# Kernel tuning notes

Measured on AMD Instinct MI355X. Metric: run time of the kernel, lower is better.

Reference implementation:

```python
import jax, jax.numpy as jnp
import numpy as np

B = 64
NS = [5024, 1257, 315, 80, 21]  # padded vertex counts per mesh level
K = 9                            # spiral length
LAT = 256


def _sconv(x, idx, W, b, elu=True):
    # x: [B, N, F], idx: [N, K] spiral neighbor indices -> gather, GEMM, activation, zero-pad mask
    Bq, N, _ = x.shape
    g = x[:, idx.reshape(-1), :].reshape(Bq, N, -1)  # [B, N, K*F]
    o = g @ W + b
    if elu:
        o = jax.nn.elu(o)
    return o.at[:, -1, :].set(0.0)  # zero the padding vertex


def _pool(M, x):
    # M: [M_out, M_in] dense down/up-sample matrix
    return jnp.einsum('mn,bnf->bmf', M, x)


def _forward(x, s0, s1, s2, s3, D0, D1, D2, D3, U0, U1, U2, U3,
             We0, be0, We1, be1, We2, be2, We3, be3,
             fceW, fceb, fcdW, fcdb,
             Wd0, bd0, Wd1, bd1, Wd2, bd2, Wd3, bd3):
    # encoder: spiral conv + downsample at each level
    h = _pool(D0, _sconv(x, s0, We0, be0))
    h = _pool(D1, _sconv(h, s1, We1, be1))
    h = _pool(D2, _sconv(h, s2, We2, be2))
    h = _pool(D3, _sconv(h, s3, We3, be3))
    z = h.reshape(h.shape[0], -1) @ fceW + fceb          # [B, LAT]
    # decoder: upsample + spiral conv, last conv has identity activation
    h = (z @ fcdW + fcdb).reshape(z.shape[0], NS[4], -1)  # [B, 21, 256]
    h = _sconv(_pool(U3, h), s3, Wd0, bd0)
    h = _sconv(_pool(U2, h), s2, Wd1, bd1)
    h = _sconv(_pool(U1, h), s1, Wd2, bd2)
    h = _sconv(_pool(U0, h), s0, Wd3, bd3, elu=False)
    return h  # [B, 5024, 3]


def setup_inputs() -> dict:
    key = jax.random.key(0)
    ks = iter(jax.random.split(key, 64))
    nrm = lambda shape, s=0.05: jax.random.normal(next(ks), shape, dtype=jnp.float32) * s
    d = {}
    d['x'] = jax.random.normal(next(ks), (B, NS[0], 3), dtype=jnp.float32)
    for i in range(4):
        n = NS[i]
        d[f's{i}'] = jax.random.randint(next(ks), (n, K), 0, n, dtype=jnp.int32).astype(jnp.int64)
    for i in range(4):
        d[f'D{i}'] = nrm((NS[i + 1], NS[i]))
        d[f'U{i}'] = nrm((NS[i], NS[i + 1]))
    enc = [(3, 64), (64, 64), (64, 128), (128, 256)]
    for i, (fi, fo) in enumerate(enc):
        d[f'We{i}'] = nrm((fi * K, fo))
        d[f'be{i}'] = jnp.zeros((fo,), jnp.float32)
    d['fceW'] = nrm((NS[4] * 256, LAT))
    d['fceb'] = jnp.zeros((LAT,), jnp.float32)
    d['fcdW'] = nrm((LAT, NS[4] * 256))
    d['fcdb'] = jnp.zeros((NS[4] * 256,), jnp.float32)
    dec = [(256, 128), (128, 64), (64, 64), (64, 3)]
    for i, (fi, fo) in enumerate(dec):
        d[f'Wd{i}'] = nrm((fi * K, fo))
        d[f'bd{i}'] = jnp.zeros((fo,), jnp.float32)
    return d


def reference(x, s0, s1, s2, s3, D0, D1, D2, D3, U0, U1, U2, U3,
              We0, be0, We1, be1, We2, be2, We3, be3,
              fceW, fceb, fcdW, fcdb,
              Wd0, bd0, Wd1, bd1, Wd2, bd2, Wd3, bd3):
    return _forward(x, s0, s1, s2, s3, D0, D1, D2, D3, U0, U1, U2, U3,
                    We0, be0, We1, be1, We2, be2, We3, be3,
                    fceW, fceb, fcdW, fcdb,
                    Wd0, bd0, Wd1, bd1, Wd2, bd2, Wd3, bd3)
```

## Files before the change

### kernel.cpp

```cpp
#include <hip/hip_runtime.h>
#include <math.h>

typedef __attribute__((ext_vector_type(8))) _Float16 half8;
typedef __attribute__((ext_vector_type(4))) float f32x4;
typedef unsigned long long u64;

#define BK 32

#define EPI_NAT  0
#define EPI_TR   1
#define EPI_FCD  2
#define EPI_OUT  3
#define EPI_PART 4

typedef const __attribute__((address_space(1))) void* gas1;
typedef __attribute__((address_space(3))) void* las3;

__device__ __forceinline__ void gl16(const void* g, void* l) {
    __builtin_amdgcn_global_load_lds((gas1)g, (las3)l, 16, 0, 0);
}
template<int N> __device__ __forceinline__ void vwait() {
    asm volatile("s_waitcnt vmcnt(%0)" :: "n"(N) : "memory");
}
__device__ __forceinline__ void barx() {
    asm volatile("" ::: "memory");
    __builtin_amdgcn_s_barrier();
    asm volatile("" ::: "memory");
}

__global__ void __launch_bounds__(256, 3) pool2_k_impl();

template<int TBM>
__global__ __launch_bounds__(256, 3) void pool2_k(
    const _Float16* __restrict__ Aw, const _Float16* __restrict__ Bw,
    _Float16* __restrict__ Cp, int M, int Np, u64 c_rs)
{
    constexpr int FM  = TBM / 32;
    constexpr int LPS = TBM / 64 + 2;

    __shared__ _Float16 sA[3][TBM][BK];
    __shared__ _Float16 sB[3][128][BK];

    const int t  = threadIdx.x;
    const int m0 = blockIdx.y * TBM;
    const int f0 = blockIdx.x * 128;
    const int lane = t & 63;
    const int wid  = t >> 6;
    const int wm = wid >> 1;
    const int wf = wid & 1;
    const int lm = lane & 15;
    const int lg = lane >> 4;

    f32x4 acc[FM][4];
    #pragma unroll
    for (int i = 0; i < FM; ++i)
        #pragma unroll
        for (int j = 0; j < 4; ++j)
            acc[i][j] = (f32x4)0.0f;

    auto stage = [&](int buf, int ks) {
        #pragma unroll
        for (int j = 0; j < TBM / 64; ++j) {
            int c   = t + j * 256;
            int row = c >> 2;
            int sw  = ((c & 3) ^ ((row >> 1) & 3)) * 8;
            int rc  = m0 + row; if (rc >= M) rc = M - 1;
            gl16(Aw + (u64)rc * Np + ks * BK + sw,
                 (_Float16*)&sA[buf][0][0] + (u64)c * 8);
        }
        #pragma unroll
        for (int j = 0; j < 2; ++j) {
            int c   = t + j * 256;
            int row = c >> 2;
            int sw  = ((c & 3) ^ ((row >> 1) & 3)) * 8;
            gl16(Bw + (u64)(f0 + row) * Np + ks * BK + sw,
                 (_Float16*)&sB[buf][0][0] + (u64)c * 8);
        }
    };

    auto compute = [&](int buf) {
        const int sa = (lg ^ ((lm >> 1) & 3)) * 8;
        half8 af[FM], bf[4];
        #pragma unroll
        for (int i = 0; i < FM; ++i)
            af[i] = *(const half8*)&sA[buf][wm * (FM * 16) + i * 16 + lm][sa];
        #pragma unroll
        for (int j = 0; j < 4; ++j)
            bf[j] = *(const half8*)&sB[buf][wf * 64 + j * 16 + lm][sa];
        #pragma unroll
        for (int i = 0; i < FM; ++i)
            #pragma unroll
            for (int j = 0; j < 4; ++j)
                acc[i][j] = __builtin_amdgcn_mfma_f32_16x16x32_f16(af[i], bf[j], acc[i][j], 0, 0, 0);
    };

    const int ke = Np / BK;
    stage(0, 0);
    if (1 < ke) stage(1, 1);
    if (2 < ke) stage(2, 2);
    int cur = 0;
    for (int ks = 0; ks < ke; ++ks) {
        int rem = ke - ks;
        if (rem >= 3)      vwait<2 * LPS>();
        else if (rem == 2) vwait<LPS>();
        else               vwait<0>();
        barx();
        compute(cur);
        barx();
        if (ks + 3 < ke) stage(cur, ks + 3);
        cur = (cur == 2) ? 0 : cur + 1;
    }

    #pragma unroll
    for (int j = 0; j < 4; ++j) {
        int fl = f0 + wf * 64 + j * 16 + lm;
        #pragma unroll
        for (int i = 0; i < FM; ++i) {
            #pragma unroll
            for (int r = 0; r < 4; ++r) {
                int m = m0 + wm * (FM * 16) + i * 16 + lg * 4 + r;
                if (m < M)
                    Cp[(u64)m * c_rs + fl] = (_Float16)acc[i][j][r];
            }
        }
    }
}

template<int AMODE, int EPI, int TBM, int TBF, int WM, int WF>
__global__ __launch_bounds__(256) void gemm_k(
    const _Float16* __restrict__ Aw, u64 a_rs,
    const int* __restrict__ idx, int FiLog,
    const _Float16* __restrict__ Bw,
    const float* __restrict__ bias,
    void* __restrict__ Cp, u64 c_rs, int Mp_out,
    int M, int Np, int F, int flags, int ksp)
{
    constexpr int FM = TBM / WM / 16;
    constexpr int FF = TBF / WF / 16;
    constexpr int LPS_A = TBM / 64;
    constexpr bool BSM = (TBF < 64);
    constexpr int LPS_B = BSM ? 0 : TBF / 64;
    constexpr int LW0 = LPS_A + (BSM ? 1 : LPS_B);
    constexpr int LWX = LPS_A + LPS_B;
    constexpr int NI = (AMODE == 1) ? TBM : 2;

    __shared__ _Float16 sA[3][TBM][BK];
    __shared__ _Float16 sB[3][TBF][BK];
    __shared__ int sIdx[NI][9];

    const int t  = threadIdx.x;
    const int b  = blockIdx.z;
    const int m0 = blockIdx.y * TBM;
    const int f0 = blockIdx.x * TBF;
    const int lane = t & 63;
    const int wid  = t >> 6;
    const int wm = wid / WF;
    const int wf = wid % WF;
    const int lm = lane & 15;
    const int lg = lane >> 4;
    const int Fi = 1 << FiLog;

    f32x4 acc[FM][FF];
    #pragma unroll
    for (int i = 0; i < FM; ++i)
        #pragma unroll
        for (int j = 0; j < FF; ++j)
            acc[i][j] = (f32x4)0.0f;

    if constexpr (AMODE == 1) {
        for (int i = t; i < TBM * 9; i += 256) {
            int r = i / 9, k = i - r * 9;
            int rc = m0 + r; if (rc >= M) rc = M - 1;
            sIdx[r][k] = idx[rc * 9 + k];
        }
        __syncthreads();
    } else if constexpr (AMODE == 5) {
        if (t < 18) {
            int r = t / 9, k = t - r * 9;
            sIdx[r][k] = idx[((m0 >> 6) + r) * 9 + k];
        }
        __syncthreads();
    }

    auto stage = [&](int buf, int ks) {
        if constexpr (AMODE != 2) {
            #pragma unroll
            for (int j = 0; j < LPS_A; ++j) {
                int c   = t + j * 256;
                int row = c >> 2;
                int sw  = ((c & 3) ^ ((row >> 1) & 3)) * 8;
                int col = ks * BK + sw;
                const _Float16* src;
                if constexpr (AMODE == 3) {
                    int rc = m0 + row; if (rc >= M) rc = M - 1;
                    src = Aw + (u64)rc * Np + col;
                } else if constexpr (AMODE == 1) {
                    int k = col >> FiLog, fi = col & (Fi - 1);
                    src = Aw + (u64)sIdx[row][k] * a_rs + b * Fi + fi;
                } else if constexpr (AMODE == 4) {
                    int k = col >> FiLog, fi = col & (Fi - 1);
                    src = Aw + (u64)k * a_rs + (m0 + row) * Fi + fi;
                } else {
                    int k = col >> FiLog, fi = col & (Fi - 1);
                    int bb = (m0 + row) & 63;
                    src = Aw + (u64)sIdx[row >> 6][k] * a_rs + bb * Fi + fi;
                }
                gl16(src, &sA[buf][row][(c & 3) * 8]);
            }
        }
        if constexpr (!BSM) {
            #pragma unroll
            for (int j = 0; j < LPS_B; ++j) {
                int c   = t + j * 256;
                int row = c >> 2;
                int sw  = ((c & 3) ^ ((row >> 1) & 3)) * 8;
                gl16(Bw + (u64)(f0 + row) * Np + ks * BK + sw, &sB[buf][row][(c & 3) * 8]);
            }
        } else {
            if (wid == 0) {
                int c   = t;
                int row = c >> 2;
                int sw  = ((c & 3) ^ ((row >> 1) & 3)) * 8;
                gl16(Bw + (u64)(f0 + row) * Np + ks * BK + sw, &sB[buf][row][(c & 3) * 8]);
            }
        }
    };

    auto compute = [&](int buf) {
        const int sa = (lg ^ ((lm >> 1) & 3)) * 8;
        half8 af[FM], bf[FF];
        #pragma unroll
        for (int i = 0; i < FM; ++i)
            af[i] = *(const half8*)&sA[buf][wm * (FM * 16) + i * 16 + lm][sa];
        #pragma unroll
        for (int j = 0; j < FF; ++j)
            bf[j] = *(const half8*)&sB[buf][wf * (FF * 16) + j * 16 + lm][sa];
        #pragma unroll
        for (int i = 0; i < FM; ++i)
            #pragma unroll
            for (int j = 0; j < FF; ++j)
                acc[i][j] = __builtin_amdgcn_mfma_f32_16x16x32_f16(af[i], bf[j], acc[i][j], 0, 0, 0);
    };

    if constexpr (AMODE == 2) {
        stage(0, 0);
        {
            int row = t >> 1;
            int base = (t & 1) * 16;
            int rg = m0 + row;
            #pragma unroll
            for (int q = 0; q < 16; ++q) {
                int n = base + q;
                _Float16 val = (_Float16)0.f;
                if (rg < M && n < 27) {
                    int k = n / 3, fi = n - k * 3;
                    val = Aw[(u64)idx[rg * 9 + k] * a_rs + b * 3 + fi];
                }
                int ch = (n >> 3) ^ ((row >> 1) & 3);
                sA[0][row][ch * 8 + (n & 7)] = val;
            }
        }
        __syncthreads();
        compute(0);
    } else {
        int kb = 0, ke = Np / BK;
        if constexpr (AMODE == 4) { kb = b * ksp; ke = kb + ksp; }
        stage(0, kb);
        if (kb + 1 < ke) stage(1, kb + 1);
        if (kb + 2 < ke) stage(2, kb + 2);
        int cur = 0;
        for (int ks = kb; ks < ke; ++ks) {
            int rem = ke - ks;
            if (rem >= 3) {
                if constexpr (LW0 == LWX) vwait<2 * LW0>();
                else { if (wid == 0) vwait<2 * LW0>(); else vwait<2 * LWX>(); }
            } else if (rem == 2) {
                if constexpr (LW0 == LWX) vwait<LW0>();
                else { if (wid == 0) vwait<LW0>(); else vwait<LWX>(); }
            } else {
                vwait<0>();
            }
            barx();
            compute(cur);
            barx();
            if (ks + 3 < ke) stage(cur, ks + 3);
            cur = (cur == 2) ? 0 : cur + 1;
        }
    }

    #pragma unroll
    for (int j = 0; j < FF; ++j) {
        int fl = f0 + wf * (FF * 16) + j * 16 + lm;
        float bv = 0.f;
        if (bias != nullptr && fl < F) bv = bias[fl];
        #pragma unroll
        for (int i = 0; i < FM; ++i) {
            #pragma unroll
            for (int r = 0; r < 4; ++r) {
                int m = m0 + wm * (FM * 16) + i * 16 + lg * 4 + r;
                float v = acc[i][j][r] + bv;
                if (flags & 1) v = (v > 0.f) ? v : expm1f(v);
                if constexpr (EPI == EPI_NAT) {
                    if (m < M && fl < F)
                        ((_Float16*)Cp)[(u64)m * c_rs + fl] = (_Float16)v;
                } else if constexpr (EPI == EPI_TR) {
                    if (m < Mp_out && fl < F) {
                        float o = (m < M && !((flags & 2) && m == M - 1)) ? v : 0.f;
                        ((_Float16*)Cp)[(u64)b * c_rs + (u64)fl * Mp_out + m] = (_Float16)o;
                    }
                } else if constexpr (EPI == EPI_FCD) {
                    if (m < M && fl < F)
                        ((_Float16*)Cp)[((u64)m * 256 + (fl & 255)) * 32 + (fl >> 8)] = (_Float16)v;
                } else if constexpr (EPI == EPI_PART) {
                    if (m < M && fl < F)
                        ((float*)Cp)[(u64)b * c_rs + (u64)m * F + fl] = v;
                } else {
                    if (m < M && fl < F) {
                        int vo = m >> 6, bb = m & 63;
                        float o = ((flags & 2) && vo == Mp_out - 1) ? 0.f : v;
                        ((float*)Cp)[((u64)bb * Mp_out + vo) * 3 + fl] = o;
                    }
                }
            }
        }
    }
}

struct CvtPtrs { const float* p[18]; };

constexpr int CV_R[18]  = {1257,5024,315,1257,80,315,21,80,  64,64,128,256,256,5376,128,64,64,16};
constexpr int CV_N[18]  = {5024,1257,1257,315,315,80,80,21,  27,576,576,1152,5376,256,2304,1152,576,576};
constexpr int CV_NP[18] = {5120,1280,1280,320,320,96,96,32,  32,576,576,1152,5376,256,2304,1152,576,576};
constexpr int CV_F[18]  = {0,0,0,0,0,0,0,0,  64,64,128,256,256,5376,128,64,64,3};

constexpr u64 cv_elems(int i) { return (u64)CV_R[i] * CV_NP[i]; }
constexpr u64 cv_off(int i) { u64 o = 0; for (int j = 0; j < i; ++j) o += (cv_elems(j) + 255) & ~(u64)255; return o; }
constexpr int cv_blk(int i) { return (int)((cv_elems(i) + 255) >> 8); }
constexpr int cv_start(int i) { int s = 0; for (int j = 0; j < i; ++j) s += cv_blk(j); return s; }

__global__ __launch_bounds__(256) void cvt_all(CvtPtrs ps, _Float16* __restrict__ dst)
{
    const int bx = blockIdx.x, t = threadIdx.x;
    #pragma unroll
    for (int i = 0; i < 18; ++i) {
        if (bx >= cv_start(i) && bx < cv_start(i + 1)) {
            const u64 e = (u64)(bx - cv_start(i)) * 256 + t;
            if (e < cv_elems(i)) {
                const int NP = CV_NP[i], N = CV_N[i], Fo = CV_F[i];
                int row = (int)(e / (u64)NP);
                int col = (int)(e - (u64)row * NP);
                float v = 0.f;
                const float* s = ps.p[i];
                if (Fo == 0) { if (col < N) v = s[(u64)row * N + col]; }
                else         { if (col < N && row < Fo) v = s[(u64)col * Fo + row]; }
                dst[cv_off(i) + e] = (_Float16)v;
            }
        }
    }
}

__global__ void cvt_x(const float* __restrict__ src, _Float16* __restrict__ dst)
{
    int i = blockIdx.x * 256 + threadIdx.x;
    if (i >= 64 * 5024 * 3) return;
    int v = i / 192;
    int r = i - v * 192;
    int b = r / 3, c = r - b * 3;
    dst[i] = (_Float16)src[((u64)b * 5024 + v) * 3 + c];
}

__global__ void reduce_fce(const float* __restrict__ part, const float* __restrict__ bias,
                           _Float16* __restrict__ z)
{
    int i = blockIdx.x * 256 + threadIdx.x;
    int fl = i & 255;
    float s = bias[fl];
    #pragma unroll
    for (int p = 0; p < 8; ++p) s += part[(u64)p * 16384 + i];
    z[i] = (_Float16)s;
}

extern "C" void kernel_launch(void* const* d_in, const int* in_sizes, int n_in,
                              void* d_out, int out_size, void* d_ws, size_t ws_size,
                              hipStream_t stream)
{
    const float* x  = (const float*)d_in[0];
    const int* s0 = (const int*)d_in[1];
    const int* s1 = (const int*)d_in[2];
    const int* s2 = (const int*)d_in[3];
    const int* s3 = (const int*)d_in[4];
    const float* be0 = (const float*)d_in[14];
    const float* be1 = (const float*)d_in[16];
    const float* be2 = (const float*)d_in[18];
    const float* be3 = (const float*)d_in[20];
    const float* fceb = (const float*)d_in[22];
    const float* fcdb = (const float*)d_in[24];
    const float* bd0 = (const float*)d_in[26];
    const float* bd1 = (const float*)d_in[28];
    const float* bd2 = (const float*)d_in[30];
    const float* bd3 = (const float*)d_in[32];

    _Float16* W = (_Float16*)d_ws;
    size_t off = 0;
    auto alloc = [&](size_t e) { size_t o = off; off += (e + 255) & ~(size_t)255; return o; };

    const size_t oActV = alloc((size_t)5024 * 4096);
    const size_t oActT = alloc((size_t)4096 * 5120);
    const size_t oZ    = alloc((size_t)64 * 256);
    const size_t oPart = alloc((size_t)8 * 64 * 256 * 2);
    const size_t oU3in = alloc((size_t)16384 * 32);
    const size_t oXp   = alloc((size_t)5024 * 192);
    const size_t oCvt  = alloc((size_t)(cv_off(17) + ((cv_elems(17) + 255) & ~(u64)255)));
    auto wofs = [&](int i) { return oCvt + (size_t)cv_off(i); };

    cvt_x<<<dim3((64 * 5024 * 3 + 255) / 256), 256, 0, stream>>>(x, W + oXp);
    {
        CvtPtrs ps;
        ps.p[0] = (const float*)d_in[5];
        ps.p[1] = (const float*)d_in[6];
        ps.p[2] = (const float*)d_in[7];
        ps.p[3] = (const float*)d_in[8];
        ps.p[4] = (const float*)d_in[9];
        ps.p[5] = (const float*)d_in[10];
        ps.p[6] = (const float*)d_in[11];
        ps.p[7] = (const float*)d_in[12];
        ps.p[8] = (const float*)d_in[13];
        ps.p[9] = (const float*)d_in[15];
        ps.p[10] = (const float*)d_in[17];
        ps.p[11] = (const float*)d_in[19];
        ps.p[12] = (const float*)d_in[21];
        ps.p[13] = (const float*)d_in[23];
        ps.p[14] = (const float*)d_in[25];
        ps.p[15] = (const float*)d_in[27];
        ps.p[16] = (const float*)d_in[29];
        ps.p[17] = (const float*)d_in[31];
        cvt_all<<<dim3(cv_start(18)), 256, 0, stream>>>(ps, W + oCvt);
    }
    hipMemsetAsync(W + oU3in, 0, (size_t)16384 * 32 * sizeof(_Float16), stream);

    #define GEMM(AM, EP, BM_, BF_, WM_, WF_, gx, gy, gz, Aw_, ars_, idx_, FiL_, Bw_, bias_, Cp_, crs_, Mp_, M_, Np_, F_, fl_, ksp_) \
        gemm_k<AM, EP, BM_, BF_, WM_, WF_><<<dim3(gx, gy, gz), 256, 0, stream>>>( \
            Aw_, ars_, idx_, FiL_, Bw_, bias_, Cp_, crs_, Mp_, M_, Np_, F_, fl_, ksp_)
    #define POOL(TBM_, gx, gy, Aw_, Bw_, Cp_, M_, Np_, crs_) \
        pool2_k<TBM_><<<dim3(gx, gy), 256, 0, stream>>>(Aw_, Bw_, Cp_, M_, Np_, crs_)

    GEMM(2, EPI_TR, 128, 64, 2, 2, 1, 40, 64, W + oXp, 192, s0, 0,
         W + wofs(8), be0, W + oActT, (u64)64 * 5120, 5120, 5024, 32, 64, 3, 0);
    POOL(64, 32, 20, W + wofs(0), W + oActT, W + oActV, 1257, 5120, 4096);
    GEMM(1, EPI_TR, 128, 64, 2, 2, 1, 10, 64, W + oActV, 4096, s1, 6,
         W + wofs(9), be1, W + oActT, (u64)64 * 1280, 1280, 1257, 576, 64, 3, 0);
    POOL(64, 32, 5, W + wofs(2), W + oActT, W + oActV, 315, 1280, 4096);
    GEMM(1, EPI_TR, 128, 64, 2, 2, 2, 3, 64, W + oActV, 4096, s2, 6,
         W + wofs(10), be2, W + oActT, (u64)128 * 320, 320, 315, 576, 128, 3, 0);
    POOL(64, 64, 2, W + wofs(4), W + oActT, W + oActV, 80, 320, 8192);
    GEMM(1, EPI_TR, 128, 64, 2, 2, 4, 1, 64, W + oActV, 8192, s3, 7,
         W + wofs(11), be3, W + oActT, (u64)256 * 96, 96, 80, 1152, 256, 3, 0);
    POOL(64, 128, 1, W + wofs(6), W + oActT, W + oActV, 21, 96, 16384);
    GEMM(4, EPI_PART, 64, 64, 2, 2, 4, 1, 8, W + oActV, 16384, nullptr, 8,
         W + wofs(12), nullptr, W + oPart, (u64)64 * 256, 0, 64, 5376, 256, 0, 21);
    reduce_fce<<<dim3(64), 256, 0, stream>>>((const float*)(W + oPart), fceb, W + oZ);
    GEMM(3, EPI_FCD, 64, 128, 2, 2, 42, 1, 1, W + oZ, 0, nullptr, 0,
         W + wofs(13), fcdb, W + oU3in, 0, 0, 64, 256, 5376, 0, 0);
    POOL(64, 128, 2, W + wofs(7), W + oU3in, W + oActV, 80, 32, 16384);
    GEMM(1, EPI_TR, 128, 64, 2, 2, 2, 1, 64, W + oActV, 16384, s3, 8,
         W + wofs(14), bd0, W + oActT, (u64)128 * 96, 96, 80, 2304, 128, 3, 0);
    POOL(64, 64, 5, W + wofs(5), W + oActT, W + oActV, 315, 96, 8192);
    GEMM(1, EPI_TR, 128, 64, 2, 2, 1, 3, 64, W + oActV, 8192, s2, 7,
         W + wofs(15), bd1, W + oActT, (u64)64 * 320, 320, 315, 1152, 64, 3, 0);
    POOL(64, 32, 20, W + wofs(3), W + oActT, W + oActV, 1257, 320, 4096);
    GEMM(1, EPI_TR, 128, 64, 2, 2, 1, 10, 64, W + oActV, 4096, s1, 6,
         W + wofs(16), bd2, W + oActT, (u64)64 * 1280, 1280, 1257, 576, 64, 3, 0);
    POOL(128, 32, 40, W + wofs(1), W + oActT, W + oActV, 5024, 1280, 4096);
    GEMM(5, EPI_OUT, 128, 16, 4, 1, 1, 2512, 1, W + oActV, 4096, s0, 6,
         W + wofs(17), bd3, d_out, 0, 5024, 321536, 576, 3, 2, 0);
    #undef GEMM
    #undef POOL
}
```

Before: 572.2 us.

## Split-K the first two encoder pools and use 128-thread blocks for level-1 convs

Adds a split-K variant of the pool GEMM that writes fp32 partials, plus a reduction kernel that sums them and converts to fp16. It is used for the D0 and D1 downsample pools, which have long K and few output tiles. The spiral-conv GEMM is now templated on thread count, and the level-1 convs run with 128-thread blocks and a 2x1 warp layout. The goal is more blocks in flight on the small-grid stages, at the cost of extra partial-buffer traffic and an additional kernel launch per split pool.

```diff
diff --git a/kernel.cpp b/kernel.cpp
--- a/kernel.cpp
+++ b/kernel.cpp
@@ -2,6 +2,7 @@
 #include <math.h>
 
 typedef __attribute__((ext_vector_type(8))) _Float16 half8;
+typedef __attribute__((ext_vector_type(4))) _Float16 half4;
 typedef __attribute__((ext_vector_type(4))) float f32x4;
 typedef unsigned long long u64;
 
@@ -28,12 +29,10 @@
     asm volatile("" ::: "memory");
 }
 
-__global__ void __launch_bounds__(256, 3) pool2_k_impl();
-
-template<int TBM>
+template<int TBM, int SPLIT>
 __global__ __launch_bounds__(256, 3) void pool2_k(
     const _Float16* __restrict__ Aw, const _Float16* __restrict__ Bw,
-    _Float16* __restrict__ Cp, int M, int Np, u64 c_rs)
+    void* __restrict__ Cp, int M, int Np, u64 c_rs, int ksp, u64 pstr)
 {
     constexpr int FM  = TBM / 32;
     constexpr int LPS = TBM / 64 + 2;
@@ -94,12 +93,13 @@
                 acc[i][j] = __builtin_amdgcn_mfma_f32_16x16x32_f16(af[i], bf[j], acc[i][j], 0, 0, 0);
     };
 
-    const int ke = Np / BK;
-    stage(0, 0);
-    if (1 < ke) stage(1, 1);
-    if (2 < ke) stage(2, 2);
+    const int kb = blockIdx.z * ksp;
+    const int ke = kb + ksp;
+    stage(0, kb);
+    if (kb + 1 < ke) stage(1, kb + 1);
+    if (kb + 2 < ke) stage(2, kb + 2);
     int cur = 0;
-    for (int ks = 0; ks < ke; ++ks) {
+    for (int ks = kb; ks < ke; ++ks) {
         int rem = ke - ks;
         if (rem >= 3)      vwait<2 * LPS>();
         else if (rem == 2) vwait<LPS>();
@@ -119,15 +119,35 @@
             #pragma unroll
             for (int r = 0; r < 4; ++r) {
                 int m = m0 + wm * (FM * 16) + i * 16 + lg * 4 + r;
-                if (m < M)
-                    Cp[(u64)m * c_rs + fl] = (_Float16)acc[i][j][r];
-            }
-        }
-    }
-}
-
-template<int AMODE, int EPI, int TBM, int TBF, int WM, int WF>
-__global__ __launch_bounds__(256) void gemm_k(
+                if (m < M) {
+                    if constexpr (SPLIT > 1)
+                        ((float*)Cp)[(u64)blockIdx.z * pstr + (u64)m * c_rs + fl] = acc[i][j][r];
+                    else
+                        ((_Float16*)Cp)[(u64)m * c_rs + fl] = (_Float16)acc[i][j][r];
+                }
+            }
+        }
+    }
+}
+
+template<int P>
+__global__ __launch_bounds__(256) void reduce_pool(
+    const float* __restrict__ part, _Float16* __restrict__ out, int total4, u64 pstr4)
+{
+    int i = blockIdx.x * 256 + threadIdx.x;
+    if (i >= total4) return;
+    f32x4 s = ((const f32x4*)part)[i];
+    #pragma unroll
+    for (int p = 1; p < P; ++p) {
+        f32x4 v = ((const f32x4*)part)[(u64)p * pstr4 + i];
+        s = s + v;
+    }
+    half4 h = {(_Float16)s[0], (_Float16)s[1], (_Float16)s[2], (_Float16)s[3]};
+    ((half4*)out)[i] = h;
+}
+
+template<int AMODE, int EPI, int NT, int TBM, int TBF, int WM, int WF>
+__global__ __launch_bounds__(NT) void gemm_k(
     const _Float16* __restrict__ Aw, u64 a_rs,
     const int* __restrict__ idx, int FiLog,
     const _Float16* __restrict__ Bw,
@@ -137,9 +157,9 @@
 {
     constexpr int FM = TBM / WM / 16;
     constexpr int FF = TBF / WF / 16;
-    constexpr int LPS_A = TBM / 64;
+    constexpr int LPS_A = TBM * 4 / NT;
     constexpr bool BSM = (TBF < 64);
-    constexpr int LPS_B = BSM ? 0 : TBF / 64;
+    constexpr int LPS_B = BSM ? 0 : TBF * 4 / NT;
     constexpr int LW0 = LPS_A + (BSM ? 1 : LPS_B);
     constexpr int LWX = LPS_A + LPS_B;
     constexpr int NI = (AMODE == 1) ? TBM : 2;
@@ -168,7 +188,7 @@
             acc[i][j] = (f32x4)0.0f;
 
     if constexpr (AMODE == 1) {
-        for (int i = t; i < TBM * 9; i += 256) {
+        for (int i = t; i < TBM * 9; i += NT) {
             int r = i / 9, k = i - r * 9;
             int rc = m0 + r; if (rc >= M) rc = M - 1;
             sIdx[r][k] = idx[rc * 9 + k];
@@ -186,7 +206,7 @@
         if constexpr (AMODE != 2) {
             #pragma unroll
             for (int j = 0; j < LPS_A; ++j) {
-                int c   = t + j * 256;
+                int c   = t + j * NT;
                 int row = c >> 2;
                 int sw  = ((c & 3) ^ ((row >> 1) & 3)) * 8;
                 int col = ks * BK + sw;
@@ -211,7 +231,7 @@
         if constexpr (!BSM) {
             #pragma unroll
             for (int j = 0; j < LPS_B; ++j) {
-                int c   = t + j * 256;
+                int c   = t + j * NT;
                 int row = c >> 2;
                 int sw  = ((c & 3) ^ ((row >> 1) & 3)) * 8;
                 gl16(Bw + (u64)(f0 + row) * Np + ks * BK + sw, &sB[buf][row][(c & 3) * 8]);
@@ -408,6 +428,7 @@
     const size_t oActT = alloc((size_t)4096 * 5120);
     const size_t oZ    = alloc((size_t)64 * 256);
     const size_t oPart = alloc((size_t)8 * 64 * 256 * 2);
+    const size_t oPP   = alloc((size_t)2 * 1257 * 4096 * 2);
     const size_t oU3in = alloc((size_t)16384 * 32);
     const size_t oXp   = alloc((size_t)5024 * 192);
     const size_t oCvt  = alloc((size_t)(cv_off(17) + ((cv_elems(17) + 255) & ~(u64)255)));
@@ -438,40 +459,46 @@
     }
     hipMemsetAsync(W + oU3in, 0, (size_t)16384 * 32 * sizeof(_Float16), stream);
 
-    #define GEMM(AM, EP, BM_, BF_, WM_, WF_, gx, gy, gz, Aw_, ars_, idx_, FiL_, Bw_, bias_, Cp_, crs_, Mp_, M_, Np_, F_, fl_, ksp_) \
-        gemm_k<AM, EP, BM_, BF_, WM_, WF_><<<dim3(gx, gy, gz), 256, 0, stream>>>( \
+    #define GEMM(AM, EP, NT_, BM_, BF_, WM_, WF_, gx, gy, gz, Aw_, ars_, idx_, FiL_, Bw_, bias_, Cp_, crs_, Mp_, M_, Np_, F_, fl_, ksp_) \
+        gemm_k<AM, EP, NT_, BM_, BF_, WM_, WF_><<<dim3(gx, gy, gz), NT_, 0, stream>>>( \
             Aw_, ars_, idx_, FiL_, Bw_, bias_, Cp_, crs_, Mp_, M_, Np_, F_, fl_, ksp_)
     #define POOL(TBM_, gx, gy, Aw_, Bw_, Cp_, M_, Np_, crs_) \
-        pool2_k<TBM_><<<dim3(gx, gy), 256, 0, stream>>>(Aw_, Bw_, Cp_, M_, Np_, crs_)
-
-    GEMM(2, EPI_TR, 128, 64, 2, 2, 1, 40, 64, W + oXp, 192, s0, 0,
+        pool2_k<TBM_, 1><<<dim3(gx, gy, 1), 256, 0, stream>>>(Aw_, Bw_, (void*)(Cp_), M_, Np_, crs_, (Np_) / BK, 0)
+
+    GEMM(2, EPI_TR, 256, 128, 64, 2, 2, 1, 40, 64, W + oXp, 192, s0, 0,
          W + wofs(8), be0, W + oActT, (u64)64 * 5120, 5120, 5024, 32, 64, 3, 0);
-    POOL(64, 32, 20, W + wofs(0), W + oActT, W + oActV, 1257, 5120, 4096);
-    GEMM(1, EPI_TR, 128, 64, 2, 2, 1, 10, 64, W + oActV, 4096, s1, 6,
+    pool2_k<128, 2><<<dim3(32, 10, 2), 256, 0, stream>>>(
+        W + wofs(0), W + oActT, (void*)(W + oPP), 1257, 5120, 4096, 80, (u64)1257 * 4096);
+    reduce_pool<2><<<dim3((1257 * 1024 + 255) / 256), 256, 0, stream>>>(
+        (const float*)(W + oPP), W + oActV, 1257 * 1024, (u64)1257 * 1024);
+    GEMM(1, EPI_TR, 128, 128, 64, 2, 1, 1, 10, 64, W + oActV, 4096, s1, 6,
          W + wofs(9), be1, W + oActT, (u64)64 * 1280, 1280, 1257, 576, 64, 3, 0);
-    POOL(64, 32, 5, W + wofs(2), W + oActT, W + oActV, 315, 1280, 4096);
-    GEMM(1, EPI_TR, 128, 64, 2, 2, 2, 3, 64, W + oActV, 4096, s2, 6,
+    pool2_k<64, 2><<<dim3(32, 5, 2), 256, 0, stream>>>(
+        W + wofs(2), W + oActT, (void*)(W + oPP), 315, 1280, 4096, 20, (u64)315 * 4096);
+    reduce_pool<2><<<dim3((315 * 1024 + 255) / 256), 256, 0, stream>>>(
+        (const float*)(W + oPP), W + oActV, 315 * 1024, (u64)315 * 1024);
+    GEMM(1, EPI_TR, 256, 128, 64, 2, 2, 2, 3, 64, W + oActV, 4096, s2, 6,
          W + wofs(10), be2, W + oActT, (u64)128 * 320, 320, 315, 576, 128, 3, 0);
     POOL(64, 64, 2, W + wofs(4), W + oActT, W + oActV, 80, 320, 8192);
-    GEMM(1, EPI_TR, 128, 64, 2, 2, 4, 1, 64, W + oActV, 8192, s3, 7,
+    GEMM(1, EPI_TR, 256, 128, 64, 2, 2, 4, 1, 64, W + oActV, 8192, s3, 7,
          W + wofs(11), be3, W + oActT, (u64)256 * 96, 96, 80, 1152, 256, 3, 0);
     POOL(64, 128, 1, W + wofs(6), W + oActT, W + oActV, 21, 96, 16384);
-    GEMM(4, EPI_PART, 64, 64, 2, 2, 4, 1, 8, W + oActV, 16384, nullptr, 8,
+    GEMM(4, EPI_PART, 256, 64, 64, 2, 2, 4, 1, 8, W + oActV, 16384, nullptr, 8,
          W + wofs(12), nullptr, W + oPart, (u64)64 * 256, 0, 64, 5376, 256, 0, 21);
     reduce_fce<<<dim3(64), 256, 0, stream>>>((const float*)(W + oPart), fceb, W + oZ);
-    GEMM(3, EPI_FCD, 64, 128, 2, 2, 42, 1, 1, W + oZ, 0, nullptr, 0,
+    GEMM(3, EPI_FCD, 256, 64, 128, 2, 2, 42, 1, 1, W + oZ, 0, nullptr, 0,
          W + wofs(13), fcdb, W + oU3in, 0, 0, 64, 256, 5376, 0, 0);
     POOL(64, 128, 2, W + wofs(7), W + oU3in, W + oActV, 80, 32, 16384);
-    GEMM(1, EPI_TR, 128, 64, 2, 2, 2, 1, 64, W + oActV, 16384, s3, 8,
+    GEMM(1, EPI_TR, 256, 128, 64, 2, 2, 2, 1, 64, W + oActV, 16384, s3, 8,
          W + wofs(14), bd0, W + oActT, (u64)128 * 96, 96, 80, 2304, 128, 3, 0);
     POOL(64, 64, 5, W + wofs(5), W + oActT, W + oActV, 315, 96, 8192);
-    GEMM(1, EPI_TR, 128, 64, 2, 2, 1, 3, 64, W + oActV, 8192, s2, 7,
+    GEMM(1, EPI_TR, 256, 128, 64, 2, 2, 1, 3, 64, W + oActV, 8192, s2, 7,
          W + wofs(15), bd1, W + oActT, (u64)64 * 320, 320, 315, 1152, 64, 3, 0);
     POOL(64, 32, 20, W + wofs(3), W + oActT, W + oActV, 1257, 320, 4096);
-    GEMM(1, EPI_TR, 128, 64, 2, 2, 1, 10, 64, W + oActV, 4096, s1, 6,
+    GEMM(1, EPI_TR, 128, 128, 64, 2, 1, 1, 10, 64, W + oActV, 4096, s1, 6,
          W + wofs(16), bd2, W + oActT, (u64)64 * 1280, 1280, 1257, 576, 64, 3, 0);
     POOL(128, 32, 40, W + wofs(1), W + oActT, W + oActV, 5024, 1280, 4096);
-    GEMM(5, EPI_OUT, 128, 16, 4, 1, 1, 2512, 1, W + oActV, 4096, s0, 6,
+    GEMM(5, EPI_OUT, 256, 128, 16, 4, 1, 1, 2512, 1, W + oActV, 4096, s0, 6,
          W + wofs(17), bd3, d_out, 0, 5024, 321536, 576, 3, 2, 0);
     #undef GEMM
     #undef POOL
```

New measurement: 606.9 us. 1.06x slower.
